# Kernel tuning notes

Hardware: AMD Instinct MI355X
Metric: run time of the kernel (lower is better)

## Reference

```python
import jax, jax.numpy as jnp
import numpy as np

N = 100000        # nodes
E = 1600000       # edges (avg degree 16)
F_IN = 128        # in_features
AH = 16           # attention_size
ALPHA = 0.2       # LeakyReLU negative slope


def setup_inputs() -> dict:
    key = jax.random.key(0)
    ks = jax.random.split(key, 10)
    xav = lambda k, shp, fan: jax.random.normal(k, shp, jnp.float32) * (1.414 * (2.0 / fan) ** 0.5)
    return {
        "input": jax.random.normal(ks[0], (N, F_IN), jnp.float32),
        "edges": jax.random.randint(ks[1], (2, E), 0, N, jnp.int32),
        "edge_factor": jax.random.normal(ks[2], (E,), jnp.float32),
        "adj_sparse_sum_rowwise": jnp.ones((N, 1), jnp.float32),
        "degree": jax.random.uniform(ks[3], (N,), jnp.float32) + 0.1,
        # Linear_2mini: in_features -> attention_hid
        "w_mini": xav(ks[4], (F_IN, AH), F_IN + AH),
        "b_mini": jnp.zeros((AH,), jnp.float32),
        "attention_bias": jnp.zeros((1, AH), jnp.float32),
        # linear_factor1: 3*AH -> AH ; linear_factor2: AH -> 1
        "lf1_w": xav(ks[5], (3 * AH, AH), 4 * AH),
        "lf1_b": jnp.zeros((AH,), jnp.float32),
        "lf2_w": xav(ks[6], (AH, 1), AH + 1),
        "lf2_b": jnp.zeros((1,), jnp.float32),
        "adj": 0,
        "iftrain": 0,
    }


def _edge_mlp(h_src, h_dst, h_diff, lf1_w, lf1_b, lf2_w, lf2_b):
    # [E, 3*AH] -> [E, AH] -> leaky_relu -> [E, 1] -> sigmoid -> [E]
    f = jnp.concatenate([h_src, h_dst, h_diff], axis=1)
    f = f @ lf1_w + lf1_b
    f = jax.nn.leaky_relu(f, ALPHA)
    f = f @ lf2_w + lf2_b
    return jax.nn.sigmoid(f[:, 0])


def reference(input, edges, edge_factor, adj_sparse_sum_rowwise, degree,
              w_mini, b_mini, attention_bias, lf1_w, lf1_b, lf2_w, lf2_b,
              adj, iftrain):
    n = input.shape[0]
    src, dst = edges[0], edges[1]

    # Linear_2mini projection [N, AH]
    new_h_mini = input @ w_mini + b_mini
    h_src = new_h_mini[src]                   # [E, AH]
    h_dst = new_h_mini[dst]                   # [E, AH]
    h_diff = jnp.abs(h_dst - h_src)           # [E, AH]

    # first edge MLP -> sigmoid factor per edge
    fc0 = _edge_mlp(h_src, h_dst, h_diff, lf1_w, lf1_b, lf2_w, lf2_b)  # [E]

    # row-wise MEAN of fc0 over edges grouped by source row (spmm reduce='mean')
    row_cnt = jax.ops.segment_sum(jnp.ones_like(fc0), src, num_segments=n)
    factor_res_1hop = jax.ops.segment_sum(fc0, src, num_segments=n) / jnp.maximum(row_cnt, 1.0)  # [N]

    factor_src = factor_res_1hop[src]         # [E]
    factor_dst = factor_res_1hop[dst]         # [E]

    # second edge MLP with attention bias added to endpoints
    fc1 = _edge_mlp(h_src + attention_bias, h_dst + attention_bias, h_diff,
                    lf1_w, lf1_b, lf2_w, lf2_b)  # [E]

    ef = factor_src * factor_dst * fc1        # new edge_factor [E]

    # row-wise SUM of edge factors (spmm with ones, reduce='sum')
    ef_row_sum = jax.ops.segment_sum(ef, src, num_segments=n)[:, None]  # [N,1]
    aggr_factor = ef_row_sum / adj_sparse_sum_rowwise                   # [N,1]

    deg = degree[:, None]                                               # [N,1]
    # sparse matmul: out[i] = sum_{e: src[e]=i} ef[e] * (input*deg)[dst[e]]
    msg = ef[:, None] * (input * deg)[dst]                              # [E, F]
    spmm = jax.ops.segment_sum(msg, src, num_segments=n)                # [N, F]

    final_h = spmm * deg + (1.0 - aggr_factor) * input
    return final_h, ef
```

## Files before the change

### kernel.cpp

```cpp
#include <hip/hip_runtime.h>
#include <math.h>

#define F_IN 128
#define AH 16
#define ALPHA 0.2f
#define NB_MAX 1024
#define TILE 4096
#define EPT 16
#define CAP 5120
#define PCAP 6144

typedef __attribute__((ext_vector_type(8))) short short8;
typedef __attribute__((ext_vector_type(4))) float f32x4;
typedef __attribute__((ext_vector_type(2))) float f32x2;

__device__ __forceinline__ unsigned f2bf_rn(float x) {
    unsigned u = __float_as_uint(x);
    return (u + 0x7fffu + ((u >> 16) & 1u)) >> 16;
}
#define LOF(u) __uint_as_float((u) << 16)
#define HIF(u) __uint_as_float((u) & 0xffff0000u)

#if __has_builtin(__builtin_amdgcn_cvt_pk_fp8_f32) && __has_builtin(__builtin_amdgcn_cvt_pk_f32_fp8)
__device__ __forceinline__ unsigned short fp8_pack2(float x, float y) {
    return (unsigned short)(__builtin_amdgcn_cvt_pk_fp8_f32(x, y, 0, false) & 0xffff);
}
__device__ __forceinline__ f32x2 fp8_unpack2(unsigned u) {
    return __builtin_amdgcn_cvt_pk_f32_fp8((int)u, false);
}
#else
__device__ __forceinline__ unsigned fp8_enc1(float x) {
    unsigned u = __float_as_uint(x);
    const unsigned s = (u >> 24) & 0x80u;
    u &= 0x7fffffffu;
    if (u < 0x3C000000u) return s;
    if (u < 0x3C800000u) return s | 0x08u;
    const unsigned r = u + 0x7ffffu + ((u >> 20) & 1u);
    const unsigned e32 = r >> 23;
    return s | (((e32 - 120u) & 0xfu) << 3) | ((r >> 20) & 7u);
}
__device__ __forceinline__ unsigned short fp8_pack2(float x, float y) {
    return (unsigned short)(fp8_enc1(x) | (fp8_enc1(y) << 8));
}
__device__ __forceinline__ float fp8_dec1(unsigned b) {
    return __uint_as_float(((b & 0x80u) << 24) | ((b & 0x7fu) << 20)) * 0x1p120f;
}
__device__ __forceinline__ f32x2 fp8_unpack2(unsigned u) {
    f32x2 r; r.x = fp8_dec1(u & 0xffu); r.y = fp8_dec1((u >> 8) & 0xffu);
    return r;
}
#endif


__global__ void k_mini(const float* __restrict__ input,
                       const float* __restrict__ w,
                       const float* __restrict__ b,
                       const float* __restrict__ degree,
                       unsigned short* __restrict__ hb,
                       unsigned short* __restrict__ simf8, int n) {
    __shared__ float ws[F_IN * AH];
    __shared__ float rows[16][F_IN + 1];
    __shared__ float dgs[16];
    for (int i = threadIdx.x; i < F_IN * AH; i += blockDim.x) ws[i] = w[i];
    const int base = blockIdx.x * 16;
    for (int idx = threadIdx.x; idx < 16 * F_IN; idx += blockDim.x) {
        const int l = idx >> 7, f = idx & 127;
        const int node = base + l;
        rows[l][f] = (node < n) ? input[(size_t)node * F_IN + f] : 0.f;
    }
    if (threadIdx.x < 16) {
        const int node = base + threadIdx.x;
        dgs[threadIdx.x] = (node < n) ? degree[node] : 0.f;
    }
    __syncthreads();
    {
        const int l = threadIdx.x >> 4;
        const int j = threadIdx.x & 15;
        const int node = base + l;
        if (node < n) {
            float acc = b[j];
            #pragma unroll 8
            for (int f = 0; f < F_IN; ++f) acc += rows[l][f] * ws[f * AH + j];
            hb[(size_t)node * AH + j] = (unsigned short)f2bf_rn(acc);
        }
    }
    for (int idx = threadIdx.x; idx < 16 * 64; idx += blockDim.x) {
        const int l = idx >> 6, pr = idx & 63;
        const int node = base + l;
        if (node < n) {
            const float dg = dgs[l];
            simf8[(size_t)node * 64 + pr] =
                fp8_pack2(rows[l][2 * pr] * dg, rows[l][2 * pr + 1] * dg);
        }
    }
}

__global__ void k_binit(int* __restrict__ bucket_cur, int nb1,
                        const float* __restrict__ lf1_w, const float* __restrict__ ab,
                        float* __restrict__ Cj) {
    for (int b = threadIdx.x; b < nb1; b += blockDim.x) bucket_cur[b] = b * CAP;
    if (threadIdx.x < AH) {
        float c = 0.f;
        for (int k = 0; k < AH; ++k)
            c += ab[k] * (lf1_w[k * AH + threadIdx.x] + lf1_w[(AH + k) * AH + threadIdx.x]);
        Cj[threadIdx.x] = c;
    }
}

__global__ __launch_bounds__(256, 4)
void k_mlp_mfma(const int* __restrict__ src, const int* __restrict__ dst,
                const unsigned short* __restrict__ hb,
                const float* __restrict__ lf1_w, const float* __restrict__ lf1_b,
                const float* __restrict__ lf2_w, const float* __restrict__ lf2_b,
                const float* __restrict__ Cj,
                unsigned* __restrict__ fcb, int e) {
    const int lane = threadIdx.x & 63;
    const int g    = lane >> 4;
    const int col  = lane & 15;

    short8 A1, A2;
    #pragma unroll
    for (int i = 0; i < 8; ++i) {
        A1[i] = (short)f2bf_rn(lf1_w[(8 * g + i) * AH + col]);
        A2[i] = (g < 2) ? (short)f2bf_rn(lf1_w[(32 + 8 * g + i) * AH + col]) : (short)0;
    }
    const f32x4 bias4 = *(const f32x4*)(lf1_b + 4 * g);
    const f32x4 cj4   = *(const f32x4*)(Cj + 4 * g);
    const f32x4 w24   = *(const f32x4*)(lf2_w + 4 * g);
    const float b2    = lf2_b[0];

    const int wid    = (blockIdx.x * blockDim.x + threadIdx.x) >> 6;
    const int nw     = (gridDim.x * blockDim.x) >> 6;
    const int nbatch = (e + 15) >> 4;
    for (int bt = wid; bt < nbatch; bt += nw) {
        const int eidx = bt * 16 + col;
        const bool ev  = (eidx < e);
        const int s = ev ? src[eidx] : 0;
        const int d = ev ? dst[eidx] : 0;
        const int rowi = (g < 2) ? s : d;
        const uint4 B1u = *(const uint4*)(hb + (size_t)rowi * AH + (g & 1) * 8);
        uint4 H;
        H.x = (unsigned)__shfl_xor((int)B1u.x, 32);
        H.y = (unsigned)__shfl_xor((int)B1u.y, 32);
        H.z = (unsigned)__shfl_xor((int)B1u.z, 32);
        H.w = (unsigned)__shfl_xor((int)B1u.w, 32);
        uint4 B2u;
        B2u.x = (f2bf_rn(fabsf(HIF(H.x) - HIF(B1u.x))) << 16) | f2bf_rn(fabsf(LOF(H.x) - LOF(B1u.x)));
        B2u.y = (f2bf_rn(fabsf(HIF(H.y) - HIF(B1u.y))) << 16) | f2bf_rn(fabsf(LOF(H.y) - LOF(B1u.y)));
        B2u.z = (f2bf_rn(fabsf(HIF(H.z) - HIF(B1u.z))) << 16) | f2bf_rn(fabsf(LOF(H.z) - LOF(B1u.z)));
        B2u.w = (f2bf_rn(fabsf(HIF(H.w) - HIF(B1u.w))) << 16) | f2bf_rn(fabsf(LOF(H.w) - LOF(B1u.w)));

        f32x4 acc = bias4;
        acc = __builtin_amdgcn_mfma_f32_16x16x32_bf16(A1, *(const short8*)&B1u, acc, 0, 0, 0);
        acc = __builtin_amdgcn_mfma_f32_16x16x32_bf16(A2, *(const short8*)&B2u, acc, 0, 0, 0);

        float p0 = 0.f, p1 = 0.f;
        #pragma unroll
        for (int r = 0; r < 4; ++r) {
            const float f  = acc[r];
            const float v0 = f > 0.f ? f : ALPHA * f;
            const float t  = f + cj4[r];
            const float v1 = t > 0.f ? t : ALPHA * t;
            p0 += w24[r] * v0;
            p1 += w24[r] * v1;
        }
        p0 += __shfl_xor(p0, 16); p1 += __shfl_xor(p1, 16);
        p0 += __shfl_xor(p0, 32); p1 += __shfl_xor(p1, 32);
        if (lane < 16 && ev) {
            const float fc0 = 1.f / (1.f + expf(-(p0 + b2)));
            const float fc1 = 1.f / (1.f + expf(-(p1 + b2)));
            fcb[eidx] = (f2bf_rn(fc1) << 16) | f2bf_rn(fc0);
        }
    }
}

__global__ __launch_bounds__(256)
void k_part1(const int* __restrict__ src, const int* __restrict__ dst,
             const unsigned* __restrict__ fcb,
             int* __restrict__ bucket_cur,
             unsigned long long* __restrict__ rec, int e, int nb1) {
    __shared__ int lhist[NB_MAX];
    __shared__ int lbase[NB_MAX];
    const int t0 = blockIdx.x * TILE;
    for (int k = threadIdx.x; k < nb1; k += 256) lhist[k] = 0;
    __syncthreads();
    int sv[EPT], rv[EPT];
    #pragma unroll
    for (int k = 0; k < EPT; ++k) {
        const int i = t0 + k * 256 + threadIdx.x;
        if (i < e) {
            const int s = src[i];
            sv[k] = s;
            rv[k] = atomicAdd(&lhist[s >> 8], 1);
        } else { sv[k] = -1; rv[k] = 0; }
    }
    __syncthreads();
    for (int k = threadIdx.x; k < nb1; k += 256) {
        const int c = lhist[k];
        lbase[k] = c ? atomicAdd(&bucket_cur[k], c) : 0;
    }
    __syncthreads();
    #pragma unroll
    for (int k = 0; k < EPT; ++k) {
        const int i = t0 + k * 256 + threadIdx.x;
        if (i < e) {
            const int s = sv[k];
            const unsigned lo = ((unsigned)(s & 255) << 24) | (unsigned)dst[i];
            rec[lbase[s >> 8] + rv[k]] = ((unsigned long long)fcb[i] << 32) | lo;
        }
    }
}

__global__ void k_bscan(const int* __restrict__ bucket_cur, int* __restrict__ base,
                        int nb1, int e) {
    __shared__ int sh[1024];
    const int t = threadIdx.x;
    const int v = (t < nb1) ? (bucket_cur[t] - t * CAP) : 0;
    sh[t] = v; __syncthreads();
    for (int off = 1; off < 1024; off <<= 1) {
        const int x = (t >= off) ? sh[t - off] : 0;
        __syncthreads();
        sh[t] += x;
        __syncthreads();
    }
    if (t < nb1) base[t] = sh[t] - v;
    if (t == nb1) base[t] = e;
}

__global__ __launch_bounds__(256)
void k_part2(const int* __restrict__ bucket_cur, const int* __restrict__ bucket_base,
             const unsigned long long* __restrict__ rec,
             unsigned long long* __restrict__ rec2,
             int* __restrict__ row_end, int* __restrict__ cnt,
             float* __restrict__ factor, int n) {
    __shared__ unsigned long long lds[PCAP];
    __shared__ int lcnt[256];
    __shared__ int sh[256];
    __shared__ float lsum[256];
    const int b = blockIdx.x;
    const int start = b * CAP;
    const int count = bucket_cur[b] - start;
    const int out0  = bucket_base[b];
    lcnt[threadIdx.x] = 0;
    lsum[threadIdx.x] = 0.f;
    __syncthreads();
    for (int k = threadIdx.x; k < count; k += 256) {
        const unsigned long long r = rec[start + k];
        if (k < PCAP) lds[k] = r;
        const int off = (int)(((unsigned)r >> 24) & 255u);
        atomicAdd(&lcnt[off], 1);
        atomicAdd(&lsum[off], __uint_as_float(((unsigned)(r >> 32) & 0xffffu) << 16));
    }
    __syncthreads();
    const int v = lcnt[threadIdx.x];
    sh[threadIdx.x] = v; __syncthreads();
    for (int off = 1; off < 256; off <<= 1) {
        const int x = (threadIdx.x >= off) ? sh[threadIdx.x - off] : 0;
        __syncthreads();
        sh[threadIdx.x] += x;
        __syncthreads();
    }
    const int inc = sh[threadIdx.x];
    const int node = (b << 8) + threadIdx.x;
    if (node < n) {
        row_end[node] = out0 + inc;
        cnt[node] = v;
        factor[node] = lsum[threadIdx.x] / fmaxf((float)v, 1.f);
    }
    lcnt[threadIdx.x] = inc - v;
    __syncthreads();
    for (int k = threadIdx.x; k < count; k += 256) {
        const unsigned long long r = (k < PCAP) ? lds[k] : rec[start + k];
        const int off = (int)(((unsigned)r >> 24) & 255u);
        const int p = out0 + atomicAdd(&lcnt[off], 1);
        rec2[p] = r;
    }
}

__global__ void k_ef(const int* __restrict__ src, const int* __restrict__ dst,
                     const unsigned* __restrict__ fcb, const float* __restrict__ factor,
                     float* __restrict__ ef_out, int e) {
    const int i = blockIdx.x * blockDim.x + threadIdx.x;
    if (i < e) {
        const unsigned fb = fcb[i];
        ef_out[i] = factor[src[i]] * factor[dst[i]] *
                    __uint_as_float(fb & 0xffff0000u);
    }
}

__global__ void k_spmm_final(const int* __restrict__ row_end, const int* __restrict__ cnt,
                             const unsigned long long* __restrict__ rec,
                             const float* __restrict__ factor,
                             const unsigned* __restrict__ simf32,
                             const float* __restrict__ input,
                             const float* __restrict__ degree,
                             const float* __restrict__ adj_row,
                             float* __restrict__ out_h, int n) {
    __shared__ float2 sh[256];
    const int wid   = (blockIdx.x * blockDim.x + threadIdx.x) >> 6;
    const int lane  = threadIdx.x & 63;
    const int half  = lane >> 5;
    const int sub   = lane & 31;
    const int sbase = threadIdx.x & ~63;
    if (wid >= n) return;
    const int end = row_end[wid];
    const int beg = end - cnt[wid];
    const float fnode = factor[wid];
    float a0 = 0.f, a1 = 0.f, a2 = 0.f, a3 = 0.f, efl = 0.f;
    for (int base = beg; base < end; base += 64) {
        const int rem = end - base;
        const int mm = rem < 64 ? rem : 64;
        float ef = 0.f; int dl = 0;
        if (lane < mm) {
            const unsigned long long r = rec[base + lane];
            const int d = (int)((unsigned)r & 0xffffffu);
            const float fc1 = __uint_as_float((unsigned)(r >> 32) & 0xffff0000u);
            ef = fnode * factor[d] * fc1;
            dl = d;
        }
        efl += ef;
        sh[sbase + lane] = make_float2(ef, __int_as_float(dl));
        for (int j = 0; j < mm; j += 8) {
            const float2 t0 = sh[sbase + j + 0 + half];
            const float2 t1 = sh[sbase + j + 2 + half];
            const float2 t2 = sh[sbase + j + 4 + half];
            const float2 t3 = sh[sbase + j + 6 + half];
            const unsigned u0 = simf32[(size_t)__float_as_int(t0.y) * 32 + sub];
            const unsigned u1 = simf32[(size_t)__float_as_int(t1.y) * 32 + sub];
            const unsigned u2 = simf32[(size_t)__float_as_int(t2.y) * 32 + sub];
            const unsigned u3 = simf32[(size_t)__float_as_int(t3.y) * 32 + sub];
            const f32x2 l0 = fp8_unpack2(u0 & 0xffffu), h0 = fp8_unpack2(u0 >> 16);
            const f32x2 l1 = fp8_unpack2(u1 & 0xffffu), h1 = fp8_unpack2(u1 >> 16);
            const f32x2 l2 = fp8_unpack2(u2 & 0xffffu), h2 = fp8_unpack2(u2 >> 16);
            const f32x2 l3 = fp8_unpack2(u3 & 0xffffu), h3 = fp8_unpack2(u3 >> 16);
            a0 += t0.x * l0.x; a1 += t0.x * l0.y; a2 += t0.x * h0.x; a3 += t0.x * h0.y;
            a0 += t1.x * l1.x; a1 += t1.x * l1.y; a2 += t1.x * h1.x; a3 += t1.x * h1.y;
            a0 += t2.x * l2.x; a1 += t2.x * l2.y; a2 += t2.x * h2.x; a3 += t2.x * h2.y;
            a0 += t3.x * l3.x; a1 += t3.x * l3.y; a2 += t3.x * h3.x; a3 += t3.x * h3.y;
        }
    }
    a0 += __shfl_xor(a0, 32);
    a1 += __shfl_xor(a1, 32);
    a2 += __shfl_xor(a2, 32);
    a3 += __shfl_xor(a3, 32);
    for (int off = 32; off > 0; off >>= 1) efl += __shfl_xor(efl, off);
    if (half == 0) {
        const float aggr = efl / adj_row[wid];
        const float dg = degree[wid];
        const float one_aggr = 1.f - aggr;
        const float4 inn = *(const float4*)(input + (size_t)wid * F_IN + 4 * sub);
        float4 o;
        o.x = a0 * dg + one_aggr * inn.x;
        o.y = a1 * dg + one_aggr * inn.y;
        o.z = a2 * dg + one_aggr * inn.z;
        o.w = a3 * dg + one_aggr * inn.w;
        *(float4*)(out_h + (size_t)wid * F_IN + 4 * sub) = o;
    }
}

extern "C" void kernel_launch(void* const* d_in, const int* in_sizes, int n_in,
                              void* d_out, int out_size, void* d_ws, size_t ws_size,
                              hipStream_t stream) {
    const float* input   = (const float*)d_in[0];
    const int*   edges   = (const int*)  d_in[1];
    const float* adj_row = (const float*)d_in[3];
    const float* degree  = (const float*)d_in[4];
    const float* w_mini  = (const float*)d_in[5];
    const float* b_mini  = (const float*)d_in[6];
    const float* ab      = (const float*)d_in[7];
    const float* lf1_w   = (const float*)d_in[8];
    const float* lf1_b   = (const float*)d_in[9];
    const float* lf2_w   = (const float*)d_in[10];
    const float* lf2_b   = (const float*)d_in[11];

    const int N = in_sizes[0] / F_IN;
    const int E = in_sizes[1] / 2;
    const int NB1 = (N + 255) >> 8;
    const int* src = edges;
    const int* dst = edges + E;

    float* final_h = (float*)d_out;
    float* ef_out  = (float*)d_out + (size_t)N * F_IN;

    unsigned short* hb  = (unsigned short*)d_ws;
    unsigned* fcb  = (unsigned*)(hb + (size_t)N * AH);
    float* factor  = (float*)(fcb + E);
    int*   cnt     = (int*)(factor + N);
    int*   row_end = cnt + N;
    float* Cj      = (float*)(row_end + N);
    int*   bucket_base = (int*)(Cj + 16);
    int*   bucket_cur  = bucket_base + NB_MAX + 1;
    unsigned long long* rec =
        (unsigned long long*)((((uintptr_t)(bucket_cur + NB_MAX)) + 15) & ~(uintptr_t)15);
    unsigned long long* rec2 = rec + (size_t)NB1 * CAP;
    unsigned short* simf8 =
        (unsigned short*)((((uintptr_t)(rec2 + E)) + 255) & ~(uintptr_t)255);

    k_mini<<<(N + 15) / 16, 256, 0, stream>>>(input, w_mini, b_mini, degree, hb, simf8, N);
    k_binit<<<1, 512, 0, stream>>>(bucket_cur, NB1, lf1_w, ab, Cj);
    k_mlp_mfma<<<4096, 256, 0, stream>>>(src, dst, hb,
                                         lf1_w, lf1_b, lf2_w, lf2_b, Cj,
                                         fcb, E);
    k_part1<<<(E + TILE - 1) / TILE, 256, 0, stream>>>(src, dst, fcb,
                                                       bucket_cur, rec, E, NB1);
    k_bscan<<<1, 1024, 0, stream>>>(bucket_cur, bucket_base, NB1, E);
    k_part2<<<NB1, 256, 0, stream>>>(bucket_cur, bucket_base, rec, rec2,
                                     row_end, cnt, factor, N);
    k_ef<<<(E + 255) / 256, 256, 0, stream>>>(src, dst, fcb, factor, ef_out, E);
    k_spmm_final<<<(N * 64 + 255) / 256, 256, 0, stream>>>(row_end, cnt, rec2, factor,
                                                           (const unsigned*)simf8,
                                                           input, degree, adj_row, final_h, N);
}
```

Baseline: 201.6 us.

## Fuse setup, ef and spmm launches and sort buckets in place without scan

The bucket init and Cj precompute move into the projection kernel. The separate bucket scan kernel and the compacted rec2 buffer are removed: each bucket is now sorted in place inside its fixed CAP-sized slot, and row_end is expressed relative to the bucket start. The ef computation becomes extra blocks of the spmm launch, and input rows are loaded as float4. This cuts the pipeline from eight launches to five and drops one full pass over the edge records, at the cost of relying on bucket counts never exceeding the LDS staging capacity.

```diff
diff --git a/kernel.cpp b/kernel.cpp
--- a/kernel.cpp
+++ b/kernel.cpp
@@ -57,16 +57,21 @@
                        const float* __restrict__ b,
                        const float* __restrict__ degree,
                        unsigned short* __restrict__ hb,
-                       unsigned short* __restrict__ simf8, int n) {
+                       unsigned short* __restrict__ simf8,
+                       int* __restrict__ bucket_cur, int nb1,
+                       const float* __restrict__ lf1_w, const float* __restrict__ ab,
+                       float* __restrict__ Cj, int n) {
     __shared__ float ws[F_IN * AH];
-    __shared__ float rows[16][F_IN + 1];
+    __shared__ float rows[16][F_IN + 4];
     __shared__ float dgs[16];
     for (int i = threadIdx.x; i < F_IN * AH; i += blockDim.x) ws[i] = w[i];
     const int base = blockIdx.x * 16;
-    for (int idx = threadIdx.x; idx < 16 * F_IN; idx += blockDim.x) {
-        const int l = idx >> 7, f = idx & 127;
+    for (int idx = threadIdx.x; idx < 16 * 32; idx += blockDim.x) {
+        const int l = idx >> 5, q = idx & 31;
         const int node = base + l;
-        rows[l][f] = (node < n) ? input[(size_t)node * F_IN + f] : 0.f;
+        float4 v = make_float4(0.f, 0.f, 0.f, 0.f);
+        if (node < n) v = *(const float4*)(input + (size_t)node * F_IN + 4 * q);
+        *(float4*)&rows[l][4 * q] = v;
     }
     if (threadIdx.x < 16) {
         const int node = base + threadIdx.x;
@@ -93,17 +98,14 @@
                 fp8_pack2(rows[l][2 * pr] * dg, rows[l][2 * pr + 1] * dg);
         }
     }
-}
-
-__global__ void k_binit(int* __restrict__ bucket_cur, int nb1,
-                        const float* __restrict__ lf1_w, const float* __restrict__ ab,
-                        float* __restrict__ Cj) {
-    for (int b = threadIdx.x; b < nb1; b += blockDim.x) bucket_cur[b] = b * CAP;
-    if (threadIdx.x < AH) {
-        float c = 0.f;
-        for (int k = 0; k < AH; ++k)
-            c += ab[k] * (lf1_w[k * AH + threadIdx.x] + lf1_w[(AH + k) * AH + threadIdx.x]);
-        Cj[threadIdx.x] = c;
+    if (blockIdx.x == 0) {
+        for (int bb = threadIdx.x; bb < nb1; bb += blockDim.x) bucket_cur[bb] = bb * CAP;
+        if (threadIdx.x < AH) {
+            float c = 0.f;
+            for (int k = 0; k < AH; ++k)
+                c += ab[k] * (lf1_w[k * AH + threadIdx.x] + lf1_w[(AH + k) * AH + threadIdx.x]);
+            Cj[threadIdx.x] = c;
+        }
     }
 }
 
@@ -211,26 +213,9 @@
     }
 }
 
-__global__ void k_bscan(const int* __restrict__ bucket_cur, int* __restrict__ base,
-                        int nb1, int e) {
-    __shared__ int sh[1024];
-    const int t = threadIdx.x;
-    const int v = (t < nb1) ? (bucket_cur[t] - t * CAP) : 0;
-    sh[t] = v; __syncthreads();
-    for (int off = 1; off < 1024; off <<= 1) {
-        const int x = (t >= off) ? sh[t - off] : 0;
-        __syncthreads();
-        sh[t] += x;
-        __syncthreads();
-    }
-    if (t < nb1) base[t] = sh[t] - v;
-    if (t == nb1) base[t] = e;
-}
-
 __global__ __launch_bounds__(256)
-void k_part2(const int* __restrict__ bucket_cur, const int* __restrict__ bucket_base,
-             const unsigned long long* __restrict__ rec,
-             unsigned long long* __restrict__ rec2,
+void k_part2(const int* __restrict__ bucket_cur,
+             unsigned long long* __restrict__ rec,
              int* __restrict__ row_end, int* __restrict__ cnt,
              float* __restrict__ factor, int n) {
     __shared__ unsigned long long lds[PCAP];
@@ -240,13 +225,12 @@
     const int b = blockIdx.x;
     const int start = b * CAP;
     const int count = bucket_cur[b] - start;
-    const int out0  = bucket_base[b];
     lcnt[threadIdx.x] = 0;
     lsum[threadIdx.x] = 0.f;
     __syncthreads();
     for (int k = threadIdx.x; k < count; k += 256) {
         const unsigned long long r = rec[start + k];
-        if (k < PCAP) lds[k] = r;
+        lds[k] = r;
         const int off = (int)(((unsigned)r >> 24) & 255u);
         atomicAdd(&lcnt[off], 1);
         atomicAdd(&lsum[off], __uint_as_float(((unsigned)(r >> 32) & 0xffffu) << 16));
@@ -263,40 +247,41 @@
     const int inc = sh[threadIdx.x];
     const int node = (b << 8) + threadIdx.x;
     if (node < n) {
-        row_end[node] = out0 + inc;
+        row_end[node] = start + inc;
         cnt[node] = v;
         factor[node] = lsum[threadIdx.x] / fmaxf((float)v, 1.f);
     }
     lcnt[threadIdx.x] = inc - v;
     __syncthreads();
     for (int k = threadIdx.x; k < count; k += 256) {
-        const unsigned long long r = (k < PCAP) ? lds[k] : rec[start + k];
+        const unsigned long long r = lds[k];
         const int off = (int)(((unsigned)r >> 24) & 255u);
-        const int p = out0 + atomicAdd(&lcnt[off], 1);
-        rec2[p] = r;
-    }
-}
-
-__global__ void k_ef(const int* __restrict__ src, const int* __restrict__ dst,
-                     const unsigned* __restrict__ fcb, const float* __restrict__ factor,
-                     float* __restrict__ ef_out, int e) {
-    const int i = blockIdx.x * blockDim.x + threadIdx.x;
-    if (i < e) {
-        const unsigned fb = fcb[i];
-        ef_out[i] = factor[src[i]] * factor[dst[i]] *
-                    __uint_as_float(fb & 0xffff0000u);
-    }
-}
-
-__global__ void k_spmm_final(const int* __restrict__ row_end, const int* __restrict__ cnt,
-                             const unsigned long long* __restrict__ rec,
-                             const float* __restrict__ factor,
-                             const unsigned* __restrict__ simf32,
-                             const float* __restrict__ input,
-                             const float* __restrict__ degree,
-                             const float* __restrict__ adj_row,
-                             float* __restrict__ out_h, int n) {
+        const int p = start + atomicAdd(&lcnt[off], 1);
+        rec[p] = r;
+    }
+}
+
+__global__ void k_spmm_ef(const int* __restrict__ row_end, const int* __restrict__ cnt,
+                          const unsigned long long* __restrict__ rec,
+                          const float* __restrict__ factor,
+                          const unsigned* __restrict__ simf32,
+                          const float* __restrict__ input,
+                          const float* __restrict__ degree,
+                          const float* __restrict__ adj_row,
+                          const int* __restrict__ src, const int* __restrict__ dst,
+                          const unsigned* __restrict__ fcb,
+                          float* __restrict__ out_h, float* __restrict__ ef_out,
+                          int n, int e, int spmm_blocks) {
     __shared__ float2 sh[256];
+    if ((int)blockIdx.x >= spmm_blocks) {
+        const int i = ((int)blockIdx.x - spmm_blocks) * 256 + threadIdx.x;
+        if (i < e) {
+            const unsigned fb = fcb[i];
+            ef_out[i] = factor[src[i]] * factor[dst[i]] *
+                        __uint_as_float(fb & 0xffff0000u);
+        }
+        return;
+    }
     const int wid   = (blockIdx.x * blockDim.x + threadIdx.x) >> 6;
     const int lane  = threadIdx.x & 63;
     const int half  = lane >> 5;
@@ -388,26 +373,26 @@
     int*   cnt     = (int*)(factor + N);
     int*   row_end = cnt + N;
     float* Cj      = (float*)(row_end + N);
-    int*   bucket_base = (int*)(Cj + 16);
-    int*   bucket_cur  = bucket_base + NB_MAX + 1;
+    int*   bucket_cur = (int*)(Cj + 16);
     unsigned long long* rec =
         (unsigned long long*)((((uintptr_t)(bucket_cur + NB_MAX)) + 15) & ~(uintptr_t)15);
-    unsigned long long* rec2 = rec + (size_t)NB1 * CAP;
     unsigned short* simf8 =
-        (unsigned short*)((((uintptr_t)(rec2 + E)) + 255) & ~(uintptr_t)255);
-
-    k_mini<<<(N + 15) / 16, 256, 0, stream>>>(input, w_mini, b_mini, degree, hb, simf8, N);
-    k_binit<<<1, 512, 0, stream>>>(bucket_cur, NB1, lf1_w, ab, Cj);
+        (unsigned short*)((((uintptr_t)(rec + (size_t)NB1 * CAP)) + 255) & ~(uintptr_t)255);
+
+    k_mini<<<(N + 15) / 16, 256, 0, stream>>>(input, w_mini, b_mini, degree, hb, simf8,
+                                              bucket_cur, NB1, lf1_w, ab, Cj, N);
     k_mlp_mfma<<<4096, 256, 0, stream>>>(src, dst, hb,
                                          lf1_w, lf1_b, lf2_w, lf2_b, Cj,
                                          fcb, E);
     k_part1<<<(E + TILE - 1) / TILE, 256, 0, stream>>>(src, dst, fcb,
                                                        bucket_cur, rec, E, NB1);
-    k_bscan<<<1, 1024, 0, stream>>>(bucket_cur, bucket_base, NB1, E);
-    k_part2<<<NB1, 256, 0, stream>>>(bucket_cur, bucket_base, rec, rec2,
-                                     row_end, cnt, factor, N);
-    k_ef<<<(E + 255) / 256, 256, 0, stream>>>(src, dst, fcb, factor, ef_out, E);
-    k_spmm_final<<<(N * 64 + 255) / 256, 256, 0, stream>>>(row_end, cnt, rec2, factor,
-                                                           (const unsigned*)simf8,
-                                                           input, degree, adj_row, final_h, N);
-}
+    k_part2<<<NB1, 256, 0, stream>>>(bucket_cur, rec, row_end, cnt, factor, N);
+    {
+        const int spmm_blocks = (N * 64 + 255) / 256;
+        const int ef_blocks   = (E + 255) / 256;
+        k_spmm_ef<<<spmm_blocks + ef_blocks, 256, 0, stream>>>(
+            row_end, cnt, rec, factor, (const unsigned*)simf8,
+            input, degree, adj_row, src, dst, fcb,
+            final_h, ef_out, N, E, spmm_blocks);
+    }
+}
```

Result: faster. 176.7 us (-12.4%).
